# Kernel optimization log

Measured on AMD Instinct MI355X. Metric: run time of the kernel, lower is better.

The kernel has to match this reference:

```python
import jax, jax.numpy as jnp
import numpy as np

DIM = 256
NUM_HEADS = 8
HEAD_DIM = DIM // NUM_HEADS
WH, WW = 7, 7
N = WH * WW              # tokens per window = 49
NUM_WINDOWS = 64         # windows per image (56x56 map / 7x7 windows)
B_TOTAL = 2048           # num_windows * B_images
SCALE = HEAD_DIM ** -0.5


def _relative_position_index():
    # Matches the tf.meshgrid (xy indexing) construction in the source.
    coords = np.stack(np.meshgrid(np.arange(WH), np.arange(WW)), axis=0)  # [2, WW, WH]
    flat = coords.reshape(2, -1)                                          # [2, N]
    rel = flat[:, :, None] - flat[:, None, :]                             # [2, N, N]
    rel = rel.transpose(1, 2, 0).astype(np.int32)                         # [N, N, 2]
    rel[:, :, 0] += WH - 1
    rel[:, :, 1] += WW - 1
    rel[:, :, 0] *= 2 * WW - 1
    return rel.sum(-1)                                                    # [N, N]


def setup_inputs() -> dict:
    key = jax.random.key(0)
    ks = jax.random.split(key, 6)
    std = 0.02
    x = jax.random.normal(ks[0], (B_TOTAL, N, DIM), dtype=jnp.float32)
    mask = jnp.zeros((NUM_WINDOWS, N, N), dtype=jnp.float32)  # 0 / -inf additive mask
    qkv_w = jax.random.normal(ks[1], (DIM, 3 * DIM), dtype=jnp.float32) * std
    qkv_b = jnp.zeros((3 * DIM,), dtype=jnp.float32)
    proj_w = jax.random.normal(ks[2], (DIM, DIM), dtype=jnp.float32) * std
    proj_b = jnp.zeros((DIM,), dtype=jnp.float32)
    n_rel = (2 * WH - 1) * (2 * WW - 1)  # 169
    bias_table = jax.random.normal(ks[3], (n_rel, NUM_HEADS), dtype=jnp.float32) * std
    rel_index = jnp.asarray(_relative_position_index(), dtype=jnp.int32)
    return {"x": x, "mask": mask, "qkv_w": qkv_w, "qkv_b": qkv_b,
            "proj_w": proj_w, "proj_b": proj_b, "bias_table": bias_table,
            "rel_index": rel_index}


def reference(x, mask, qkv_w, qkv_b, proj_w, proj_b, bias_table, rel_index):
    B = x.shape[0]
    # qkv projection -> [3, B, H, N, hd]
    qkv = x @ qkv_w + qkv_b                                  # [B, N, 3C]
    qkv = qkv.reshape(B, N, 3, NUM_HEADS, HEAD_DIM)
    qkv = jnp.transpose(qkv, (2, 0, 3, 1, 4))
    q, k, v = qkv[0], qkv[1], qkv[2]
    # scaled attention scores [B, H, N, N]
    attn = jnp.einsum('bhnd,bhmd->bhnm', q, k) * SCALE
    # relative position bias gather: [N*N] -> [N, N, H] -> [1, H, N, N]
    bias = bias_table[rel_index.reshape(-1)].reshape(N, N, NUM_HEADS)
    attn = attn + jnp.transpose(bias, (2, 0, 1))[None]
    # additive window mask [nW, N, N]
    nW = mask.shape[0]
    attn = attn.reshape(B // nW, nW, NUM_HEADS, N, N) + mask[None, :, None]
    attn = attn.reshape(B, NUM_HEADS, N, N)
    attn = jax.nn.softmax(attn, axis=-1)
    out = jnp.einsum('bhnm,bhmd->bhnd', attn, v)             # [B, H, N, hd]
    out = jnp.transpose(out, (0, 2, 1, 3)).reshape(B, N, DIM)
    return out @ proj_w + proj_b
```

## Files before the change

kernel.cpp:

```cpp
#include <hip/hip_runtime.h>

#define NTOK 49
#define NHEAD 8
#define HDIM 32
#define DIMC 256
#define SCALE_F 0.17677669529663687f

typedef __attribute__((ext_vector_type(8))) short short8;
typedef __attribute__((ext_vector_type(4))) float f32x4;

#define AS1P(p) ((__attribute__((address_space(1))) void*)(p))
#define AS3P(p) ((__attribute__((address_space(3))) void*)(p))

__device__ inline unsigned short f2bf(float f) {
    unsigned int u = __float_as_uint(f);
    u += 0x7fffu + ((u >> 16) & 1u);
    return (unsigned short)(u >> 16);
}

__global__ __launch_bounds__(256) void conv_pack(const float* __restrict__ in,
    unsigned short* __restrict__ xp, int M)
{
    __shared__ __align__(16) unsigned short T[32 * 64 * 8];
    const int t = threadIdx.x;
    const size_t m0 = (size_t)blockIdx.x * 64;
    const float* src = in + m0 * 256;
    #pragma unroll
    for (int i = 0; i < 8; ++i) {
        const int li = i * 256 + t;
        const int r  = li >> 5;
        const int kc = li & 31;
        float4 a = ((const float4*)src)[li * 2];
        float4 b = ((const float4*)src)[li * 2 + 1];
        union { unsigned short s[8]; uint4 v; } u;
        u.s[0] = f2bf(a.x); u.s[1] = f2bf(a.y); u.s[2] = f2bf(a.z); u.s[3] = f2bf(a.w);
        u.s[4] = f2bf(b.x); u.s[5] = f2bf(b.y); u.s[6] = f2bf(b.z); u.s[7] = f2bf(b.w);
        *(uint4*)(T + kc * 512 + ((r ^ (kc & 7)) * 8)) = u.v;
    }
    __syncthreads();
    #pragma unroll
    for (int j = 0; j < 8; ++j) {
        const int li = j * 256 + t;
        const int kc = li >> 6;
        const int r  = li & 63;
        uint4 v = *(const uint4*)(T + kc * 512 + ((r ^ (kc & 7)) * 8));
        *(uint4*)(xp + ((size_t)kc * M + m0 + r) * 8) = v;
    }
}

__global__ __launch_bounds__(256) void pack_w(const float* __restrict__ W,
    unsigned short* __restrict__ Wp, int K, int N)
{
    int idx = blockIdx.x * 256 + threadIdx.x;
    if (idx >= K * N) return;
    int k = idx / N, n = idx - k * N;
    Wp[((size_t)(k >> 3) * N + n) * 8 + (k & 7)] = f2bf(W[idx]);
}

__global__ __launch_bounds__(256) void bm_build(const float* __restrict__ bias_table,
    const int* __restrict__ rel_index, const float* __restrict__ mask,
    float* __restrict__ bm)
{
    int idx = blockIdx.x * 256 + threadIdx.x;
    if (idx >= 64 * NHEAD * NTOK * NTOK) return;
    int wh = idx / (NTOK * NTOK);
    int ij = idx - wh * (NTOK * NTOK);
    int w = wh >> 3, h = wh & 7;
    bm[idx] = bias_table[rel_index[ij] * NHEAD + h] + mask[(size_t)w * (NTOK * NTOK) + ij];
}

template <bool OUT_BF16>
__global__ __launch_bounds__(256) void gemm_mfma(
    const unsigned short* __restrict__ Ap,
    const unsigned short* __restrict__ Wp,
    const float* __restrict__ Bv,
    void* __restrict__ Yv,
    int N, int M, int nbm)
{
    __shared__ __align__(16) unsigned short As[4096];
    __shared__ __align__(16) unsigned short Bs[4096];

    const int tid  = threadIdx.x;
    const int lane = tid & 63;
    const int wv   = tid >> 6;
    const int quad = lane >> 4;
    const int l15  = lane & 15;

    const int nbn = N >> 7;
    const int lin = blockIdx.x;
    int mblk, nblk;
    if ((nbm & 7) == 0) {
        const int xcd = lin & 7;
        const int g   = lin >> 3;
        const int gm  = g / nbn;
        mblk = xcd * (nbm >> 3) + gm;
        nblk = g - gm * nbn;
    } else {
        mblk = lin / nbn;
        nblk = lin - mblk * nbn;
    }
    const long m0 = (long)mblk * 128;
    const int  n0 = nblk * 128;
    const int  wm = (wv >> 1) * 64;
    const int  wn = (wv & 1) * 64;

    const unsigned short* ga0 = Ap + ((size_t)wv * M + m0 + lane) * 8;
    const unsigned short* ga1 = ga0 + 64 * 8;
    const unsigned short* gb0 = Wp + ((size_t)wv * N + n0 + lane) * 8;
    const unsigned short* gb1 = gb0 + 64 * 8;

    f32x4 acc[4][4];
    #pragma unroll
    for (int i = 0; i < 4; ++i)
        #pragma unroll
        for (int j = 0; j < 4; ++j) acc[i][j] = (f32x4){0.f, 0.f, 0.f, 0.f};

    for (int k0 = 0; k0 < 256; k0 += 32) {
        const size_t aofs = (size_t)(k0 >> 3) * M * 8;
        const size_t bofs = (size_t)(k0 >> 3) * N * 8;
        __builtin_amdgcn_global_load_lds(AS1P(ga0 + aofs), AS3P(As + wv * 1024),       16, 0, 0);
        __builtin_amdgcn_global_load_lds(AS1P(ga1 + aofs), AS3P(As + wv * 1024 + 512), 16, 0, 0);
        __builtin_amdgcn_global_load_lds(AS1P(gb0 + bofs), AS3P(Bs + wv * 1024),       16, 0, 0);
        __builtin_amdgcn_global_load_lds(AS1P(gb1 + bofs), AS3P(Bs + wv * 1024 + 512), 16, 0, 0);
        __syncthreads();
        short8 af[4], bq[4];
        #pragma unroll
        for (int t = 0; t < 4; ++t) {
            af[t] = *(const short8*)(As + quad * 1024 + (wm + t * 16 + l15) * 8);
            bq[t] = *(const short8*)(Bs + quad * 1024 + (wn + t * 16 + l15) * 8);
        }
        #pragma unroll
        for (int ti = 0; ti < 4; ++ti)
            #pragma unroll
            for (int tj = 0; tj < 4; ++tj)
                acc[ti][tj] = __builtin_amdgcn_mfma_f32_16x16x32_bf16(bq[tj], af[ti], acc[ti][tj], 0, 0, 0);
        __syncthreads();
    }

    float4 bv4[4];
    #pragma unroll
    for (int tj = 0; tj < 4; ++tj)
        bv4[tj] = *(const float4*)(Bv + n0 + wn + tj * 16 + quad * 4);

    #pragma unroll
    for (int ti = 0; ti < 4; ++ti) {
        const long row = m0 + wm + ti * 16 + l15;
        #pragma unroll
        for (int tj = 0; tj < 4; ++tj) {
            const int col = n0 + wn + tj * 16 + quad * 4;
            const float v0 = acc[ti][tj][0] + bv4[tj].x;
            const float v1 = acc[ti][tj][1] + bv4[tj].y;
            const float v2 = acc[ti][tj][2] + bv4[tj].z;
            const float v3 = acc[ti][tj][3] + bv4[tj].w;
            if (OUT_BF16) {
                uint2 u;
                u.x = (unsigned int)f2bf(v0) | ((unsigned int)f2bf(v1) << 16);
                u.y = (unsigned int)f2bf(v2) | ((unsigned int)f2bf(v3) << 16);
                *(uint2*)((unsigned short*)Yv + row * N + col) = u;
            } else {
                float4 o = {v0, v1, v2, v3};
                *(float4*)((float*)Yv + row * N + col) = o;
            }
        }
    }
}

__global__ __launch_bounds__(128) void attn_mfma(
    const unsigned short* __restrict__ qkvb,
    const float* __restrict__ bm,
    unsigned short* __restrict__ o1b,
    int win0, int Mc)
{
    __shared__ __align__(16) unsigned short SMEM[2 * 3528];

    const int wvid = threadIdx.x >> 6;
    const int lane = threadIdx.x & 63;
    const int h    = blockIdx.x * 2 + wvid;
    const int b    = blockIdx.y;
    const int w    = (win0 + b) & 63;
    const int quad = lane >> 4;
    const int l15  = lane & 15;

    unsigned short* Vt = SMEM + wvid * 3528;
    unsigned short* Ps = SMEM + wvid * 3528;
    unsigned short* Os = SMEM + wvid * 3528;

    const unsigned short* wbase = qkvb + (size_t)b * NTOK * 768 + h * HDIM;

    {
        const int tok = (lane < NTOK) ? lane : (NTOK - 1);
        const unsigned short* vp = wbase + (size_t)tok * 768 + 512;
        #pragma unroll
        for (int c = 0; c < 4; ++c) {
            uint4 vv = *(const uint4*)(vp + c * 8);
            unsigned int uu[4] = {vv.x, vv.y, vv.z, vv.w};
            #pragma unroll
            for (int e = 0; e < 4; ++e) {
                int d = c * 8 + e * 2;
                Vt[d * 72 + lane]       = (unsigned short)(uu[e] & 0xffffu);
                Vt[(d + 1) * 72 + lane] = (unsigned short)(uu[e] >> 16);
            }
        }
    }

    short8 aq[4], bk[4];
    #pragma unroll
    for (int t = 0; t < 4; ++t) {
        int row = t * 16 + l15; if (row >= NTOK) row = NTOK - 1;
        const unsigned short* rp = wbase + (size_t)row * 768 + quad * 8;
        aq[t] = *(const short8*)(rp);
        bk[t] = *(const short8*)(rp + 256);
    }

    f32x4 sa[4][4];
    #pragma unroll
    for (int ti = 0; ti < 4; ++ti)
        #pragma unroll
        for (int tj = 0; tj < 4; ++tj) {
            f32x4 z = (f32x4){0.f, 0.f, 0.f, 0.f};
            sa[ti][tj] = __builtin_amdgcn_mfma_f32_16x16x32_bf16(aq[ti], bk[tj], z, 0, 0, 0);
        }

    short8 vb2[2][2];
    #pragma unroll
    for (int td = 0; td < 2; ++td)
        #pragma unroll
        for (int kc = 0; kc < 2; ++kc)
            vb2[td][kc] = *(const short8*)(Vt + (td * 16 + l15) * 72 + kc * 32 + quad * 8);

    const float* bmb = bm + (size_t)(w * NHEAD + h) * (NTOK * NTOK);
    float inv[4][4];
    #pragma unroll
    for (int ti = 0; ti < 4; ++ti) {
        #pragma unroll
        for (int r = 0; r < 4; ++r) {
            const int row = ti * 16 + quad * 4 + r;
            float sv[4];
            #pragma unroll
            for (int tj = 0; tj < 4; ++tj) {
                const int col = tj * 16 + l15;
                float s;
                if (col < NTOK) {
                    float add = (row < NTOK) ? bmb[row * NTOK + col] : 0.f;
                    s = sa[ti][tj][r] * SCALE_F + add;
                } else {
                    s = -__builtin_inff();
                }
                sv[tj] = s;
            }
            float e0 = __expf(sv[0]), e1 = __expf(sv[1]);
            float e2 = __expf(sv[2]), e3 = __expf(sv[3]);
            sa[ti][0][r] = e0; sa[ti][1][r] = e1; sa[ti][2][r] = e2; sa[ti][3][r] = e3;
            float sum = (e0 + e1) + (e2 + e3);
            sum += __shfl_xor(sum, 1, 16);
            sum += __shfl_xor(sum, 2, 16);
            sum += __shfl_xor(sum, 4, 16);
            sum += __shfl_xor(sum, 8, 16);
            inv[ti][r] = 1.f / sum;
        }
    }

    __syncthreads();

    #pragma unroll
    for (int ti = 0; ti < 4; ++ti)
        #pragma unroll
        for (int r = 0; r < 4; ++r) {
            const int row = ti * 16 + quad * 4 + r;
            if (row < NTOK) {
                #pragma unroll
                for (int tj = 0; tj < 4; ++tj)
                    Ps[row * 72 + tj * 16 + l15] = f2bf(sa[ti][tj][r]);
            }
        }

    short8 pa[4][2];
    #pragma unroll
    for (int ti = 0; ti < 4; ++ti) {
        int row = ti * 16 + l15; if (row >= NTOK) row = NTOK - 1;
        #pragma unroll
        for (int kc = 0; kc < 2; ++kc)
            pa[ti][kc] = *(const short8*)(Ps + row * 72 + kc * 32 + quad * 8);
    }
    f32x4 oa[4][2];
    #pragma unroll
    for (int ti = 0; ti < 4; ++ti)
        #pragma unroll
        for (int td = 0; td < 2; ++td) {
            f32x4 z = (f32x4){0.f, 0.f, 0.f, 0.f};
            z = __builtin_amdgcn_mfma_f32_16x16x32_bf16(pa[ti][0], vb2[td][0], z, 0, 0, 0);
            oa[ti][td] = __builtin_amdgcn_mfma_f32_16x16x32_bf16(pa[ti][1], vb2[td][1], z, 0, 0, 0);
        }

    #pragma unroll
    for (int ti = 0; ti < 4; ++ti)
        #pragma unroll
        for (int r = 0; r < 4; ++r) {
            const int row = ti * 16 + quad * 4 + r;
            if (row < NTOK) {
                const float si = inv[ti][r];
                #pragma unroll
                for (int td = 0; td < 2; ++td) {
                    const int d = td * 16 + l15;
                    Os[(d >> 3) * (NTOK * 8) + row * 8 + (d & 7)] =
                        f2bf(oa[ti][td][r] * si);
                }
            }
        }

    if (lane < NTOK) {
        #pragma unroll
        for (int kg = 0; kg < 4; ++kg) {
            uint4 v = *(const uint4*)(Os + kg * (NTOK * 8) + lane * 8);
            *(uint4*)(o1b + ((size_t)(h * 4 + kg) * Mc + (size_t)b * NTOK + lane) * 8) = v;
        }
    }
}

extern "C" void kernel_launch(void* const* d_in, const int* in_sizes, int n_in,
                              void* d_out, int out_size, void* d_ws, size_t ws_size,
                              hipStream_t stream)
{
    const float* x          = (const float*)d_in[0];
    const float* mask       = (const float*)d_in[1];
    const float* qkv_w      = (const float*)d_in[2];
    const float* qkv_b      = (const float*)d_in[3];
    const float* proj_w     = (const float*)d_in[4];
    const float* proj_b     = (const float*)d_in[5];
    const float* bias_table = (const float*)d_in[6];
    const int*   rel_index  = (const int*)d_in[7];
    float* outp = (float*)d_out;

    const int B_TOTAL = 2048;
    char* ws = (char*)d_ws;
    size_t off = 0;
    auto carve = [&](size_t bytes) -> void* {
        void* p = ws + off; off += (bytes + 255) & ~(size_t)255; return p;
    };
    unsigned short* WpQ = (unsigned short*)carve((size_t)256 * 768 * 2);
    unsigned short* WpP = (unsigned short*)carve((size_t)256 * 256 * 2);
    float* bm = (float*)carve((size_t)64 * NHEAD * NTOK * NTOK * 4);
    const size_t fixed = off;
    const size_t PER_WIN = (size_t)NTOK * 256 * 2 + (size_t)NTOK * 768 * 2 + (size_t)NTOK * 256 * 2;
    size_t avail = (ws_size > fixed + 1024) ? (ws_size - fixed - 1024) : 0;
    int chunkW = (int)(avail / PER_WIN);
    if (chunkW > B_TOTAL) chunkW = B_TOTAL;
    chunkW &= ~127;
    if (chunkW < 128) chunkW = 128;
    unsigned short* x_bf = (unsigned short*)carve((size_t)chunkW * NTOK * 256 * 2);
    unsigned short* qkvb = (unsigned short*)carve((size_t)chunkW * NTOK * 768 * 2);
    unsigned short* o1b  = (unsigned short*)carve((size_t)chunkW * NTOK * 256 * 2);

    pack_w<<<(256 * 768 + 255) / 256, 256, 0, stream>>>(qkv_w, WpQ, 256, 768);
    pack_w<<<(256 * 256 + 255) / 256, 256, 0, stream>>>(proj_w, WpP, 256, 256);
    bm_build<<<(64 * NHEAD * NTOK * NTOK + 255) / 256, 256, 0, stream>>>(
        bias_table, rel_index, mask, bm);

    for (int w0 = 0; w0 < B_TOTAL; w0 += chunkW) {
        int wc = B_TOTAL - w0; if (wc > chunkW) wc = chunkW;
        const int Mc = wc * NTOK;
        const int nbm = Mc / 128;
        conv_pack<<<Mc / 64, 256, 0, stream>>>(
            x + (size_t)w0 * NTOK * DIMC, x_bf, Mc);
        gemm_mfma<true ><<<dim3(nbm * 6), 256, 0, stream>>>(x_bf, WpQ, qkv_b, qkvb, 768, Mc, nbm);
        attn_mfma<<<dim3(NHEAD / 2, wc), 128, 0, stream>>>(qkvb, bm, o1b, w0, Mc);
        gemm_mfma<false><<<dim3(nbm * 2), 256, 0, stream>>>(
            o1b, WpP, proj_b, outp + (size_t)w0 * NTOK * DIMC, 256, Mc, nbm);
    }
}
```

Before: 389.4 us.

## Fuse output projection into window attention kernel, dropping intermediate buffer

The attention kernel now handles one whole window per 256-thread block, with four waves each covering two heads. It writes the attention output into LDS in packed layout and then runs the 256x256 output projection in the same kernel, streaming the projection weights from global memory. This removes the o1b global round trip and the separate projection GEMM launch. In exchange each block uses more LDS, which can lower occupancy, and each block re-reads the full projection weight matrix.

After: 448.0 us. 15.0% more time.

```diff
diff --git a/kernel.cpp b/kernel.cpp
--- a/kernel.cpp
+++ b/kernel.cpp
@@ -69,12 +69,11 @@
     bm[idx] = bias_table[rel_index[ij] * NHEAD + h] + mask[(size_t)w * (NTOK * NTOK) + ij];
 }
 
-template <bool OUT_BF16>
 __global__ __launch_bounds__(256) void gemm_mfma(
     const unsigned short* __restrict__ Ap,
     const unsigned short* __restrict__ Wp,
     const float* __restrict__ Bv,
-    void* __restrict__ Yv,
+    unsigned short* __restrict__ Yv,
     int N, int M, int nbm)
 {
     __shared__ __align__(16) unsigned short As[4096];
@@ -148,171 +147,218 @@
         #pragma unroll
         for (int tj = 0; tj < 4; ++tj) {
             const int col = n0 + wn + tj * 16 + quad * 4;
-            const float v0 = acc[ti][tj][0] + bv4[tj].x;
-            const float v1 = acc[ti][tj][1] + bv4[tj].y;
-            const float v2 = acc[ti][tj][2] + bv4[tj].z;
-            const float v3 = acc[ti][tj][3] + bv4[tj].w;
-            if (OUT_BF16) {
-                uint2 u;
-                u.x = (unsigned int)f2bf(v0) | ((unsigned int)f2bf(v1) << 16);
-                u.y = (unsigned int)f2bf(v2) | ((unsigned int)f2bf(v3) << 16);
-                *(uint2*)((unsigned short*)Yv + row * N + col) = u;
-            } else {
-                float4 o = {v0, v1, v2, v3};
-                *(float4*)((float*)Yv + row * N + col) = o;
-            }
-        }
-    }
-}
-
-__global__ __launch_bounds__(128) void attn_mfma(
+            uint2 u;
+            u.x = (unsigned int)f2bf(acc[ti][tj][0] + bv4[tj].x)
+                | ((unsigned int)f2bf(acc[ti][tj][1] + bv4[tj].y) << 16);
+            u.y = (unsigned int)f2bf(acc[ti][tj][2] + bv4[tj].z)
+                | ((unsigned int)f2bf(acc[ti][tj][3] + bv4[tj].w) << 16);
+            *(uint2*)(Yv + row * N + col) = u;
+        }
+    }
+}
+
+__global__ __launch_bounds__(256) void attn_proj(
     const unsigned short* __restrict__ qkvb,
     const float* __restrict__ bm,
-    unsigned short* __restrict__ o1b,
-    int win0, int Mc)
-{
-    __shared__ __align__(16) unsigned short SMEM[2 * 3528];
-
-    const int wvid = threadIdx.x >> 6;
+    const unsigned short* __restrict__ WpP,
+    const float* __restrict__ Pb,
+    float* __restrict__ outp,
+    int win0)
+{
+    __shared__ __align__(16) unsigned short SMEM[4 * 3528 + 32 * 64 * 8];
+
+    const int wv   = threadIdx.x >> 6;
     const int lane = threadIdx.x & 63;
-    const int h    = blockIdx.x * 2 + wvid;
-    const int b    = blockIdx.y;
+    const int b    = blockIdx.x;
     const int w    = (win0 + b) & 63;
     const int quad = lane >> 4;
     const int l15  = lane & 15;
 
-    unsigned short* Vt = SMEM + wvid * 3528;
-    unsigned short* Ps = SMEM + wvid * 3528;
-    unsigned short* Os = SMEM + wvid * 3528;
-
-    const unsigned short* wbase = qkvb + (size_t)b * NTOK * 768 + h * HDIM;
-
-    {
-        const int tok = (lane < NTOK) ? lane : (NTOK - 1);
-        const unsigned short* vp = wbase + (size_t)tok * 768 + 512;
-        #pragma unroll
-        for (int c = 0; c < 4; ++c) {
-            uint4 vv = *(const uint4*)(vp + c * 8);
-            unsigned int uu[4] = {vv.x, vv.y, vv.z, vv.w};
-            #pragma unroll
-            for (int e = 0; e < 4; ++e) {
-                int d = c * 8 + e * 2;
-                Vt[d * 72 + lane]       = (unsigned short)(uu[e] & 0xffffu);
-                Vt[(d + 1) * 72 + lane] = (unsigned short)(uu[e] >> 16);
-            }
-        }
-    }
-
-    short8 aq[4], bk[4];
-    #pragma unroll
-    for (int t = 0; t < 4; ++t) {
-        int row = t * 16 + l15; if (row >= NTOK) row = NTOK - 1;
-        const unsigned short* rp = wbase + (size_t)row * 768 + quad * 8;
-        aq[t] = *(const short8*)(rp);
-        bk[t] = *(const short8*)(rp + 256);
-    }
-
-    f32x4 sa[4][4];
-    #pragma unroll
-    for (int ti = 0; ti < 4; ++ti)
-        #pragma unroll
-        for (int tj = 0; tj < 4; ++tj) {
-            f32x4 z = (f32x4){0.f, 0.f, 0.f, 0.f};
-            sa[ti][tj] = __builtin_amdgcn_mfma_f32_16x16x32_bf16(aq[ti], bk[tj], z, 0, 0, 0);
-        }
-
-    short8 vb2[2][2];
-    #pragma unroll
-    for (int td = 0; td < 2; ++td)
-        #pragma unroll
-        for (int kc = 0; kc < 2; ++kc)
-            vb2[td][kc] = *(const short8*)(Vt + (td * 16 + l15) * 72 + kc * 32 + quad * 8);
-
-    const float* bmb = bm + (size_t)(w * NHEAD + h) * (NTOK * NTOK);
-    float inv[4][4];
+    unsigned short* Vt    = SMEM + wv * 3528;
+    unsigned short* Ps    = SMEM + wv * 3528;
+    unsigned short* O_lds = SMEM + 4 * 3528;
+
+    #pragma unroll 1
+    for (int hp = 0; hp < 2; ++hp) {
+        const int h = wv * 2 + hp;
+        const unsigned short* wbase = qkvb + (size_t)b * NTOK * 768 + h * HDIM;
+
+        {
+            const int tok = (lane < NTOK) ? lane : (NTOK - 1);
+            const unsigned short* vp = wbase + (size_t)tok * 768 + 512;
+            #pragma unroll
+            for (int c = 0; c < 4; ++c) {
+                uint4 vv = *(const uint4*)(vp + c * 8);
+                unsigned int uu[4] = {vv.x, vv.y, vv.z, vv.w};
+                #pragma unroll
+                for (int e = 0; e < 4; ++e) {
+                    int d = c * 8 + e * 2;
+                    Vt[d * 72 + lane]       = (unsigned short)(uu[e] & 0xffffu);
+                    Vt[(d + 1) * 72 + lane] = (unsigned short)(uu[e] >> 16);
+                }
+            }
+        }
+
+        short8 aq[4], bk[4];
+        #pragma unroll
+        for (int t = 0; t < 4; ++t) {
+            int row = t * 16 + l15; if (row >= NTOK) row = NTOK - 1;
+            const unsigned short* rp = wbase + (size_t)row * 768 + quad * 8;
+            aq[t] = *(const short8*)(rp);
+            bk[t] = *(const short8*)(rp + 256);
+        }
+
+        f32x4 sa[4][4];
+        #pragma unroll
+        for (int ti = 0; ti < 4; ++ti)
+            #pragma unroll
+            for (int tj = 0; tj < 4; ++tj) {
+                f32x4 z = (f32x4){0.f, 0.f, 0.f, 0.f};
+                sa[ti][tj] = __builtin_amdgcn_mfma_f32_16x16x32_bf16(aq[ti], bk[tj], z, 0, 0, 0);
+            }
+
+        short8 vb2[2][2];
+        #pragma unroll
+        for (int td = 0; td < 2; ++td)
+            #pragma unroll
+            for (int kc = 0; kc < 2; ++kc)
+                vb2[td][kc] = *(const short8*)(Vt + (td * 16 + l15) * 72 + kc * 32 + quad * 8);
+
+        const float* bmb = bm + (size_t)(w * NHEAD + h) * (NTOK * NTOK);
+        float inv[4][4];
+        #pragma unroll
+        for (int ti = 0; ti < 4; ++ti) {
+            #pragma unroll
+            for (int r = 0; r < 4; ++r) {
+                const int row = ti * 16 + quad * 4 + r;
+                float sv[4];
+                #pragma unroll
+                for (int tj = 0; tj < 4; ++tj) {
+                    const int col = tj * 16 + l15;
+                    float s;
+                    if (col < NTOK) {
+                        float add = (row < NTOK) ? bmb[row * NTOK + col] : 0.f;
+                        s = sa[ti][tj][r] * SCALE_F + add;
+                    } else {
+                        s = -__builtin_inff();
+                    }
+                    sv[tj] = s;
+                }
+                float e0 = __expf(sv[0]), e1 = __expf(sv[1]);
+                float e2 = __expf(sv[2]), e3 = __expf(sv[3]);
+                sa[ti][0][r] = e0; sa[ti][1][r] = e1; sa[ti][2][r] = e2; sa[ti][3][r] = e3;
+                float sum = (e0 + e1) + (e2 + e3);
+                sum += __shfl_xor(sum, 1, 16);
+                sum += __shfl_xor(sum, 2, 16);
+                sum += __shfl_xor(sum, 4, 16);
+                sum += __shfl_xor(sum, 8, 16);
+                inv[ti][r] = 1.f / sum;
+            }
+        }
+
+        __syncthreads();
+
+        #pragma unroll
+        for (int ti = 0; ti < 4; ++ti)
+            #pragma unroll
+            for (int r = 0; r < 4; ++r) {
+                const int row = ti * 16 + quad * 4 + r;
+                if (row < NTOK) {
+                    #pragma unroll
+                    for (int tj = 0; tj < 4; ++tj)
+                        Ps[row * 72 + tj * 16 + l15] = f2bf(sa[ti][tj][r]);
+                }
+            }
+
+        short8 pa[4][2];
+        #pragma unroll
+        for (int ti = 0; ti < 4; ++ti) {
+            int row = ti * 16 + l15; if (row >= NTOK) row = NTOK - 1;
+            #pragma unroll
+            for (int kc = 0; kc < 2; ++kc)
+                pa[ti][kc] = *(const short8*)(Ps + row * 72 + kc * 32 + quad * 8);
+        }
+        f32x4 oa[4][2];
+        #pragma unroll
+        for (int ti = 0; ti < 4; ++ti)
+            #pragma unroll
+            for (int td = 0; td < 2; ++td) {
+                f32x4 z = (f32x4){0.f, 0.f, 0.f, 0.f};
+                z = __builtin_amdgcn_mfma_f32_16x16x32_bf16(pa[ti][0], vb2[td][0], z, 0, 0, 0);
+                oa[ti][td] = __builtin_amdgcn_mfma_f32_16x16x32_bf16(pa[ti][1], vb2[td][1], z, 0, 0, 0);
+            }
+
+        #pragma unroll
+        for (int ti = 0; ti < 4; ++ti)
+            #pragma unroll
+            for (int r = 0; r < 4; ++r) {
+                const int row = ti * 16 + quad * 4 + r;
+                if (row < NTOK) {
+                    const float si = inv[ti][r];
+                    #pragma unroll
+                    for (int td = 0; td < 2; ++td) {
+                        const int d = td * 16 + l15;
+                        const int kc = h * 4 + (d >> 3);
+                        O_lds[((size_t)kc * 64 + row) * 8 + (d & 7)] =
+                            f2bf(oa[ti][td][r] * si);
+                    }
+                }
+            }
+    }
+
+    __syncthreads();
+
+    const int wn = wv * 64;
+    f32x4 pacc[4][4];
+    #pragma unroll
+    for (int i = 0; i < 4; ++i)
+        #pragma unroll
+        for (int j = 0; j < 4; ++j) pacc[i][j] = (f32x4){0.f, 0.f, 0.f, 0.f};
+
+    short8 pbq[4];
+    #pragma unroll
+    for (int t = 0; t < 4; ++t)
+        pbq[t] = *(const short8*)(WpP + ((size_t)quad * 256 + wn + t * 16 + l15) * 8);
+
+    #pragma unroll
+    for (int K0 = 0; K0 < 8; ++K0) {
+        short8 af[4], bq[4];
+        #pragma unroll
+        for (int t = 0; t < 4; ++t)
+            af[t] = *(const short8*)(O_lds + ((size_t)(K0 * 4 + quad) * 64 + t * 16 + l15) * 8);
+        #pragma unroll
+        for (int t = 0; t < 4; ++t) bq[t] = pbq[t];
+        if (K0 < 7) {
+            #pragma unroll
+            for (int t = 0; t < 4; ++t)
+                pbq[t] = *(const short8*)(WpP + ((size_t)((K0 + 1) * 4 + quad) * 256 + wn + t * 16 + l15) * 8);
+        }
+        #pragma unroll
+        for (int ti = 0; ti < 4; ++ti)
+            #pragma unroll
+            for (int tj = 0; tj < 4; ++tj)
+                pacc[ti][tj] = __builtin_amdgcn_mfma_f32_16x16x32_bf16(bq[tj], af[ti], pacc[ti][tj], 0, 0, 0);
+    }
+
+    float4 bv4[4];
+    #pragma unroll
+    for (int tj = 0; tj < 4; ++tj)
+        bv4[tj] = *(const float4*)(Pb + wn + tj * 16 + quad * 4);
+
+    float* obase = outp + (size_t)b * NTOK * 256;
     #pragma unroll
     for (int ti = 0; ti < 4; ++ti) {
-        #pragma unroll
-        for (int r = 0; r < 4; ++r) {
-            const int row = ti * 16 + quad * 4 + r;
-            float sv[4];
+        const int row = ti * 16 + l15;
+        if (row < NTOK) {
             #pragma unroll
             for (int tj = 0; tj < 4; ++tj) {
-                const int col = tj * 16 + l15;
-                float s;
-                if (col < NTOK) {
-                    float add = (row < NTOK) ? bmb[row * NTOK + col] : 0.f;
-                    s = sa[ti][tj][r] * SCALE_F + add;
-                } else {
-                    s = -__builtin_inff();
-                }
-                sv[tj] = s;
-            }
-            float e0 = __expf(sv[0]), e1 = __expf(sv[1]);
-            float e2 = __expf(sv[2]), e3 = __expf(sv[3]);
-            sa[ti][0][r] = e0; sa[ti][1][r] = e1; sa[ti][2][r] = e2; sa[ti][3][r] = e3;
-            float sum = (e0 + e1) + (e2 + e3);
-            sum += __shfl_xor(sum, 1, 16);
-            sum += __shfl_xor(sum, 2, 16);
-            sum += __shfl_xor(sum, 4, 16);
-            sum += __shfl_xor(sum, 8, 16);
-            inv[ti][r] = 1.f / sum;
-        }
-    }
-
-    __syncthreads();
-
-    #pragma unroll
-    for (int ti = 0; ti < 4; ++ti)
-        #pragma unroll
-        for (int r = 0; r < 4; ++r) {
-            const int row = ti * 16 + quad * 4 + r;
-            if (row < NTOK) {
-                #pragma unroll
-                for (int tj = 0; tj < 4; ++tj)
-                    Ps[row * 72 + tj * 16 + l15] = f2bf(sa[ti][tj][r]);
-            }
-        }
-
-    short8 pa[4][2];
-    #pragma unroll
-    for (int ti = 0; ti < 4; ++ti) {
-        int row = ti * 16 + l15; if (row >= NTOK) row = NTOK - 1;
-        #pragma unroll
-        for (int kc = 0; kc < 2; ++kc)
-            pa[ti][kc] = *(const short8*)(Ps + row * 72 + kc * 32 + quad * 8);
-    }
-    f32x4 oa[4][2];
-    #pragma unroll
-    for (int ti = 0; ti < 4; ++ti)
-        #pragma unroll
-        for (int td = 0; td < 2; ++td) {
-            f32x4 z = (f32x4){0.f, 0.f, 0.f, 0.f};
-            z = __builtin_amdgcn_mfma_f32_16x16x32_bf16(pa[ti][0], vb2[td][0], z, 0, 0, 0);
-            oa[ti][td] = __builtin_amdgcn_mfma_f32_16x16x32_bf16(pa[ti][1], vb2[td][1], z, 0, 0, 0);
-        }
-
-    #pragma unroll
-    for (int ti = 0; ti < 4; ++ti)
-        #pragma unroll
-        for (int r = 0; r < 4; ++r) {
-            const int row = ti * 16 + quad * 4 + r;
-            if (row < NTOK) {
-                const float si = inv[ti][r];
-                #pragma unroll
-                for (int td = 0; td < 2; ++td) {
-                    const int d = td * 16 + l15;
-                    Os[(d >> 3) * (NTOK * 8) + row * 8 + (d & 7)] =
-                        f2bf(oa[ti][td][r] * si);
-                }
-            }
-        }
-
-    if (lane < NTOK) {
-        #pragma unroll
-        for (int kg = 0; kg < 4; ++kg) {
-            uint4 v = *(const uint4*)(Os + kg * (NTOK * 8) + lane * 8);
-            *(uint4*)(o1b + ((size_t)(h * 4 + kg) * Mc + (size_t)b * NTOK + lane) * 8) = v;
+                const int col = wn + tj * 16 + quad * 4;
+                float4 o = {pacc[ti][tj][0] + bv4[tj].x,
+                            pacc[ti][tj][1] + bv4[tj].y,
+                            pacc[ti][tj][2] + bv4[tj].z,
+                            pacc[ti][tj][3] + bv4[tj].w};
+                *(float4*)(obase + (size_t)row * 256 + col) = o;
+            }
         }
     }
 }
@@ -341,7 +387,7 @@
     unsigned short* WpP = (unsigned short*)carve((size_t)256 * 256 * 2);
     float* bm = (float*)carve((size_t)64 * NHEAD * NTOK * NTOK * 4);
     const size_t fixed = off;
-    const size_t PER_WIN = (size_t)NTOK * 256 * 2 + (size_t)NTOK * 768 * 2 + (size_t)NTOK * 256 * 2;
+    const size_t PER_WIN = (size_t)NTOK * 256 * 2 + (size_t)NTOK * 768 * 2;
     size_t avail = (ws_size > fixed + 1024) ? (ws_size - fixed - 1024) : 0;
     int chunkW = (int)(avail / PER_WIN);
     if (chunkW > B_TOTAL) chunkW = B_TOTAL;
@@ -349,7 +395,6 @@
     if (chunkW < 128) chunkW = 128;
     unsigned short* x_bf = (unsigned short*)carve((size_t)chunkW * NTOK * 256 * 2);
     unsigned short* qkvb = (unsigned short*)carve((size_t)chunkW * NTOK * 768 * 2);
-    unsigned short* o1b  = (unsigned short*)carve((size_t)chunkW * NTOK * 256 * 2);
 
     pack_w<<<(256 * 768 + 255) / 256, 256, 0, stream>>>(qkv_w, WpQ, 256, 768);
     pack_w<<<(256 * 256 + 255) / 256, 256, 0, stream>>>(proj_w, WpP, 256, 256);
@@ -362,9 +407,8 @@
         const int nbm = Mc / 128;
         conv_pack<<<Mc / 64, 256, 0, stream>>>(
             x + (size_t)w0 * NTOK * DIMC, x_bf, Mc);
-        gemm_mfma<true ><<<dim3(nbm * 6), 256, 0, stream>>>(x_bf, WpQ, qkv_b, qkvb, 768, Mc, nbm);
-        attn_mfma<<<dim3(NHEAD / 2, wc), 128, 0, stream>>>(qkvb, bm, o1b, w0, Mc);
-        gemm_mfma<false><<<dim3(nbm * 2), 256, 0, stream>>>(
-            o1b, WpP, proj_b, outp + (size_t)w0 * NTOK * DIMC, 256, Mc, nbm);
-    }
-}
+        gemm_mfma<<<dim3(nbm * 6), 256, 0, stream>>>(x_bf, WpQ, qkv_b, qkvb, 768, Mc, nbm);
+        attn_proj<<<dim3(wc), 256, 0, stream>>>(
+            qkvb, bm, WpP, proj_b, outp + (size_t)w0 * NTOK * DIMC, w0);
+    }
+}
```
